# Kernel tuning notes

Measured on AMD Instinct MI355X. Metric: run time of the kernel, lower is better.

The kernel has to match this reference:

```python
import jax, jax.numpy as jnp
import numpy as np

B, S, D, H = 2, 2048, 1024, 16
DK = D // H
NEG = -65504.0  # matches torch masked_fill value in source


def setup_inputs() -> dict:
    key = jax.random.key(0)
    ks = jax.random.split(key, 5)
    scale = 1.0 / np.sqrt(D)
    return {
        "x": jax.random.normal(ks[0], (B, S, D), dtype=jnp.float32),
        "W_q": jax.random.normal(ks[1], (D, D), dtype=jnp.float32) * scale,
        "W_k": jax.random.normal(ks[2], (D, D), dtype=jnp.float32) * scale,
        "W_v": jax.random.normal(ks[3], (D, D), dtype=jnp.float32) * scale,
        "W_o": jax.random.normal(ks[4], (D, D), dtype=jnp.float32) * scale,
    }


def reference(x, W_q, W_k, W_v, W_o):
    b, s, d = x.shape
    # nn.Linear(x) = x @ W.T ; split heads -> [b, h, s, dk]
    def proj(W):
        return (x @ W.T).reshape(b, s, H, DK).transpose(0, 2, 1, 3)
    q, k, v = proj(W_q), proj(W_k), proj(W_v)
    scores = jnp.einsum("bhqd,bhkd->bhqk", q, k) / jnp.sqrt(jnp.float32(DK))
    causal = jnp.tril(jnp.ones((s, s), dtype=bool))  # True where attending allowed
    scores = jnp.where(causal, scores, NEG)
    attn = jax.nn.softmax(scores, axis=-1)  # attn_pdrop=0 -> dropout is identity
    out = jnp.einsum("bhqk,bhkd->bhqd", attn, v)
    out = out.transpose(0, 2, 1, 3).reshape(b, s, d)
    return out @ W_o.T
```

## Files before the change

kernel.cpp:

```cpp
#include <hip/hip_runtime.h>
#include <hip/hip_bf16.h>

typedef __attribute__((ext_vector_type(4))) float f32x4;
typedef __attribute__((ext_vector_type(8))) short bf16x8;

#define Bn 2
#define Sn 2048
#define Dn 1024
#define Hn 16
#define DKn 64
#define Mrows (Bn * Sn)

__device__ __forceinline__ unsigned short f2bf(float f) {
  unsigned int x = __float_as_uint(f);
  x += 0x7fffu + ((x >> 16) & 1u);
  return (unsigned short)(x >> 16);
}

__device__ __forceinline__ float bf2f(unsigned short u) {
  return __uint_as_float(((unsigned int)u) << 16);
}

__device__ __forceinline__ unsigned int cvtpk(float lo, float hi) {
  unsigned int r;
  asm("v_cvt_pk_bf16_f32 %0, %1, %2" : "=v"(r) : "v"(lo), "v"(hi));
  return r;
}

__device__ __forceinline__ float exp2a(float x) {
  float r;
  asm("v_exp_f32 %0, %1" : "=v"(r) : "v"(x));
  return r;
}

__device__ __forceinline__ f32x4 mfma16(bf16x8 a, bf16x8 b, f32x4 c) {
  return __builtin_amdgcn_mfma_f32_16x16x32_bf16(a, b, c, 0, 0, 0);
}

__device__ __forceinline__ f32x4 max4(f32x4 a, f32x4 b) {
  f32x4 r;
  r[0] = fmaxf(a[0], b[0]); r[1] = fmaxf(a[1], b[1]);
  r[2] = fmaxf(a[2], b[2]); r[3] = fmaxf(a[3], b[3]);
  return r;
}

__device__ __forceinline__ void gload_lds16(const unsigned short* g, unsigned short* l) {
  __builtin_amdgcn_global_load_lds(
      (const __attribute__((address_space(1))) void*)g,
      (__attribute__((address_space(3))) void*)l, 16, 0, 0);
}

__global__ __launch_bounds__(256)
void cvt_all(const float* __restrict__ x,  const float* __restrict__ wq,
             const float* __restrict__ wk, const float* __restrict__ wv,
             const float* __restrict__ wo,
             unsigned short* __restrict__ xb,  unsigned short* __restrict__ wqb,
             unsigned short* __restrict__ wkb, unsigned short* __restrict__ wvb,
             unsigned short* __restrict__ wob) {
  int i = (blockIdx.x * 256 + threadIdx.x) * 4;
  const float* src; unsigned short* dst; int off;
  int r = i >> 20;
  if (r < 4)       { src = x;  dst = xb;  off = i; }
  else if (r == 4) { src = wq; dst = wqb; off = i & 1048575; }
  else if (r == 5) { src = wk; dst = wkb; off = i & 1048575; }
  else if (r == 6) { src = wv; dst = wvb; off = i & 1048575; }
  else             { src = wo; dst = wob; off = i & 1048575; }
  float4 v = *(const float4*)(src + off);
  ushort4 o;
  o.x = f2bf(v.x); o.y = f2bf(v.y); o.z = f2bf(v.z); o.w = f2bf(v.w);
  *(ushort4*)(dst + off) = o;
}

template<int MODE>
__device__ __forceinline__ void gemm_body(const unsigned short* __restrict__ A,
                                          const unsigned short* __restrict__ W,
                                          unsigned short* __restrict__ Cb,
                                          float* __restrict__ Cf,
                                          unsigned short* As,
                                          unsigned short* Bs,
                                          int row0, int col0) {
  const int K = Dn, N = Dn;
  const int tid  = threadIdx.x;
  const int wid  = tid >> 6;
  const int lane = tid & 63;
  const int l15  = lane & 15;
  const int lg   = lane >> 4;
  const int wr = (wid >> 1) * 64;
  const int wc = (wid & 1) * 64;

  f32x4 acc[4][4] = {};

  const int lrow2 = lane >> 2;
  const int gs    = (lane & 3) ^ ((lane >> 3) & 3);
  const int swzr  = (l15 >> 1) & 3;

  auto stage = [&](int kt, int b) {
#pragma unroll
    for (int q = 0; q < 2; ++q) {
      int chunk = wid * 2 + q;
      int r = chunk * 16 + lrow2;
      gload_lds16(A + (size_t)(row0 + r) * K + kt + gs * 8,
                  &As[b * 4096 + chunk * 512]);
    }
#pragma unroll
    for (int q = 0; q < 2; ++q) {
      int chunk = wid * 2 + q;
      int r = chunk * 16 + lrow2;
      gload_lds16(W + (size_t)(col0 + r) * K + kt + gs * 8,
                  &Bs[b * 4096 + chunk * 512]);
    }
  };

  auto compute = [&](int b) {
    bf16x8 af[4], bfr[4];
#pragma unroll
    for (int m = 0; m < 4; ++m)
      af[m] = *(const bf16x8*)(&As[b * 4096 + (wr + m * 16 + l15) * 32 +
                                   ((lg ^ swzr) * 8)]);
#pragma unroll
    for (int n = 0; n < 4; ++n)
      bfr[n] = *(const bf16x8*)(&Bs[b * 4096 + (wc + n * 16 + l15) * 32 +
                                    ((lg ^ swzr) * 8)]);
    __builtin_amdgcn_s_setprio(1);
#pragma unroll
    for (int m = 0; m < 4; ++m)
#pragma unroll
      for (int n = 0; n < 4; ++n)
        acc[m][n] = mfma16(af[m], bfr[n], acc[m][n]);
    __builtin_amdgcn_s_setprio(0);
  };

  stage(0, 0);
  stage(32, 1);
  int cb = 0;
#pragma unroll 1
  for (int t = 0; t < 32; ++t) {
    if (t < 31) asm volatile("s_waitcnt vmcnt(4)" ::: "memory");
    else        asm volatile("s_waitcnt vmcnt(0)" ::: "memory");
    __builtin_amdgcn_sched_barrier(0);
    __builtin_amdgcn_s_barrier();
    __builtin_amdgcn_sched_barrier(0);
    if (t <= 29) {
      int sb = cb + 2; if (sb >= 3) sb -= 3;
      stage((t + 2) * 32, sb);
    }
    compute(cb);
    ++cb; if (cb == 3) cb = 0;
  }

#pragma unroll
  for (int m = 0; m < 4; ++m)
#pragma unroll
    for (int n = 0; n < 4; ++n) {
      int r0 = row0 + wr + m * 16 + lg * 4;
      int c  = col0 + wc + n * 16 + l15;
      if (MODE == 2) {
        int b = r0 >> 11, s = r0 & 2047;
        int h = c >> 6,  d = c & 63;
        ushort4 pw;
        pw.x = f2bf(acc[m][n][0]); pw.y = f2bf(acc[m][n][1]);
        pw.z = f2bf(acc[m][n][2]); pw.w = f2bf(acc[m][n][3]);
        *(ushort4*)(Cb + ((((size_t)b * Hn + h) * DKn + d) << 11) + s) = pw;
      } else {
#pragma unroll
        for (int j = 0; j < 4; ++j) {
          size_t idx = (size_t)(r0 + j) * N + c;
          float v = acc[m][n][j];
          if (MODE == 3)      Cf[idx] = v;
          else if (MODE == 0) Cb[idx] = f2bf(v * 0.18033688f);
          else                Cb[idx] = f2bf(v);
        }
      }
    }
}

__global__ __launch_bounds__(256, 3)
void gemm_qkv(const unsigned short* __restrict__ A,
              const unsigned short* __restrict__ W0,
              const unsigned short* __restrict__ W1,
              const unsigned short* __restrict__ W2,
              unsigned short* __restrict__ C0,
              unsigned short* __restrict__ C1,
              unsigned short* __restrict__ C2) {
  __shared__ unsigned short As[3 * 128 * 32];
  __shared__ unsigned short Bs[3 * 128 * 32];
  const int fid = blockIdx.x;
  const int panel = fid % 24;
  const int row0 = (fid / 24) * 128;
  const int col0 = (panel & 7) * 128;
  const int z = panel >> 3;
  if (z == 0)      gemm_body<0>(A, W0, C0, nullptr, As, Bs, row0, col0);
  else if (z == 1) gemm_body<1>(A, W1, C1, nullptr, As, Bs, row0, col0);
  else             gemm_body<2>(A, W2, C2, nullptr, As, Bs, row0, col0);
}

__global__ __launch_bounds__(256, 3)
void gemm_out(const unsigned short* __restrict__ A,
              const unsigned short* __restrict__ W,
              float* __restrict__ C) {
  __shared__ unsigned short As[3 * 128 * 32];
  __shared__ unsigned short Bs[3 * 128 * 32];
  gemm_body<3>(A, W, nullptr, C, As, Bs, blockIdx.x * 128, blockIdx.y * 128);
}

__global__ __launch_bounds__(512, 4)
void attn_part(const unsigned short* __restrict__ Qg,
               const unsigned short* __restrict__ Kg,
               const unsigned short* __restrict__ Vtg,
               unsigned short* __restrict__ Og,
               unsigned short* __restrict__ Pb,
               float* __restrict__ Pml) {
  const int bid = blockIdx.x;
  const int bh = bid & 31;
  const int j  = bid >> 5;
  const int bb = bh >> 4, hh = bh & 15;
  const int tid = threadIdx.x, wid = tid >> 6, lane = tid & 63;
  const int l15 = lane & 15, lg = lane >> 4;
  const int wq = wid * 16;
  const size_t baseQ = (size_t)bb * Sn * Dn + (size_t)hh * DKn;
  const size_t baseV = (size_t)bh * DKn * Sn;

  __shared__ unsigned short Ks[2][64 * 64];
  __shared__ unsigned short Vts[3][64 * 64];
  __shared__ unsigned short Ps[8][16 * 72];

  const int lrow  = lane >> 3;
  const int sgran = (lane & 7) ^ lrow;
  const int swz   = l15 & 7;

  const int g0 = 17 * j;
  int qtC = 0;
  while ((qtC + 1) * (qtC + 2) <= g0) ++qtC;
  int ktC = g0 - qtC * (qtC + 1);
  int qtN = qtC, ktN = ktC;
  { ++ktN; if (ktN == 2 * qtN + 2) { ktN = 0; ++qtN; } }
  int sqt = qtC, skt = ktC;
  int snum = 0;

  auto stage = [&]() {
    const int k0 = skt << 6;
    const int ksl = snum & 1, vsl = snum % 3;
    gload_lds16(Kg + baseQ + (size_t)(k0 + wid * 8 + lrow) * Dn + sgran * 8,
                &Ks[ksl][wid * 512]);
    gload_lds16(Vtg + baseV + (size_t)(wid * 8 + lrow) * Sn + k0 + sgran * 8,
                &Vts[vsl][wid * 512]);
    ++snum;
    ++skt; if (skt == 2 * sqt + 2) { skt = 0; ++sqt; }
  };

  bf16x8 qf[2];
  auto loadQ = [&](int qtile) {
    const int q0 = qtile * 128;
#pragma unroll
    for (int kd = 0; kd < 2; ++kd)
      qf[kd] = *(const bf16x8*)(Qg + baseQ +
               (size_t)(q0 + wq + l15) * Dn + kd * 32 + lg * 8);
  };

  f32x4 sfA[4], sfB[4];
  f32x4 oacc[4] = {};
  float mrun = -1e30f;
  float lrun = 0.f;
  int pstart = ktC;

  stage(); stage();
  loadQ(qtC);
  asm volatile("s_waitcnt vmcnt(0)" ::: "memory");
  __builtin_amdgcn_sched_barrier(0);
  __builtin_amdgcn_s_barrier();
  if ((ktC << 6) <= qtC * 128 + wq + 15) {
#pragma unroll
    for (int kn = 0; kn < 4; ++kn) sfA[kn] = f32x4{0.f, 0.f, 0.f, 0.f};
    __builtin_amdgcn_s_setprio(1);
#pragma unroll
    for (int kn = 0; kn < 4; ++kn)
#pragma unroll
      for (int kd = 0; kd < 2; ++kd) {
        bf16x8 kf = *(const bf16x8*)(&Ks[0][(kn * 16 + l15) * 64 +
                                          (((kd * 4 + lg) ^ swz) * 8)]);
        sfA[kn] = mfma16(kf, qf[kd], sfA[kn]);
      }
    __builtin_amdgcn_s_setprio(0);
  }

  auto body = [&](int i, f32x4 (&sfC)[4], f32x4 (&sfN)[4]) {
    asm volatile("s_waitcnt vmcnt(0)" ::: "memory");
    __builtin_amdgcn_sched_barrier(0);
    __builtin_amdgcn_s_barrier();
    if (i <= 14) stage();

    if (i < 16) {
      if (ktN == 0) loadQ(qtN);
      const int k0n = ktN << 6;
      if (k0n <= qtN * 128 + wq + 15) {
        const int ksl = (i + 1) & 1;
#pragma unroll
        for (int kn = 0; kn < 4; ++kn) sfN[kn] = f32x4{0.f, 0.f, 0.f, 0.f};
        __builtin_amdgcn_s_setprio(1);
#pragma unroll
        for (int kn = 0; kn < 4; ++kn)
#pragma unroll
          for (int kd = 0; kd < 2; ++kd) {
            bf16x8 kf = *(const bf16x8*)(&Ks[ksl][(kn * 16 + l15) * 64 +
                                                 (((kd * 4 + lg) ^ swz) * 8)]);
            sfN[kn] = mfma16(kf, qf[kd], sfN[kn]);
          }
        __builtin_amdgcn_s_setprio(0);
      }
    }

    const int k0c = ktC << 6;
    const int q0c = qtC * 128;
    if (k0c <= q0c + wq + 15) {
      if (k0c + 63 > q0c + wq) {
        int qq = q0c + wq + l15;
#pragma unroll
        for (int kn = 0; kn < 4; ++kn)
#pragma unroll
          for (int jj = 0; jj < 4; ++jj) {
            int key = k0c + kn * 16 + lg * 4 + jj;
            if (key > qq) sfC[kn][jj] = -1e30f;
          }
      }
      f32x4 mm = max4(max4(sfC[0], sfC[1]), max4(sfC[2], sfC[3]));
      float tl = fmaxf(fmaxf(mm[0], mm[1]), fmaxf(mm[2], mm[3]));
      if (__any(tl > mrun + 11.5f)) {
        float t = tl;
        t = fmaxf(t, __shfl_xor(t, 16));
        t = fmaxf(t, __shfl_xor(t, 32));
        float mnew = fmaxf(mrun, t);
        float corr = exp2a(mrun - mnew);
        mrun = mnew;
        lrun *= corr;
#pragma unroll
        for (int dn = 0; dn < 4; ++dn) oacc[dn] *= corr;
      }
      const float m = mrun;
#pragma unroll
      for (int kn = 0; kn < 4; ++kn) {
#pragma unroll
        for (int jj = 0; jj < 4; ++jj)
          sfC[kn][jj] = exp2a(sfC[kn][jj] - m);
        uint2 pw;
        pw.x = cvtpk(sfC[kn][0], sfC[kn][1]);
        pw.y = cvtpk(sfC[kn][2], sfC[kn][3]);
        *(uint2*)(&Ps[wid][l15 * 72 + kn * 16 + lg * 4]) = pw;
      }
      f32x4 sv = (sfC[0] + sfC[1]) + (sfC[2] + sfC[3]);
      lrun += (sv[0] + sv[1]) + (sv[2] + sv[3]);

      const int vsl = i % 3;
      __builtin_amdgcn_s_setprio(1);
#pragma unroll
      for (int kk = 0; kk < 2; ++kk) {
        bf16x8 pf = *(const bf16x8*)(&Ps[wid][l15 * 72 + kk * 32 + lg * 8]);
#pragma unroll
        for (int dn = 0; dn < 4; ++dn) {
          bf16x8 vf = *(const bf16x8*)(&Vts[vsl][(dn * 16 + l15) * 64 +
                                                (((kk * 4 + lg) ^ swz) * 8)]);
          oacc[dn] = mfma16(vf, pf, oacc[dn]);
        }
      }
      __builtin_amdgcn_s_setprio(0);
    }

    const bool segend = (ktC == 2 * qtC + 1);
    if (segend || i == 16) {
      if (pstart == 0 && segend) {
        float lt = lrun;
        lt += __shfl_xor(lt, 16);
        lt += __shfl_xor(lt, 32);
        float rinv = 1.0f / lt;
        int row = q0c + wq + l15;
#pragma unroll
        for (int dn = 0; dn < 4; ++dn) {
          ushort4 ow;
          ow.x = f2bf(oacc[dn][0] * rinv);
          ow.y = f2bf(oacc[dn][1] * rinv);
          ow.z = f2bf(oacc[dn][2] * rinv);
          ow.w = f2bf(oacc[dn][3] * rinv);
          *(ushort4*)(Og + baseQ + (size_t)row * Dn + dn * 16 + lg * 4) = ow;
        }
      } else {
        const int seg_s = qtC * (qtC + 1);
        const int ord = pstart ? ((seg_s + pstart) / 17 - seg_s / 17) : 0;
        const size_t slot = (size_t)((bh * 16 + qtC) * 3 + ord);
        float lt = lrun;
        lt += __shfl_xor(lt, 16);
        lt += __shfl_xor(lt, 32);
        int rl = wq + l15;
#pragma unroll
        for (int dn = 0; dn < 4; ++dn) {
          ushort4 ow;
          ow.x = f2bf(oacc[dn][0]);
          ow.y = f2bf(oacc[dn][1]);
          ow.z = f2bf(oacc[dn][2]);
          ow.w = f2bf(oacc[dn][3]);
          *(ushort4*)(Pb + slot * 8192 + (size_t)rl * 64 + dn * 16 + lg * 4) = ow;
        }
        if (lg == 0) {
          Pml[slot * 256 + rl] = mrun;
          Pml[slot * 256 + 128 + rl] = lt;
        }
      }
      if (i < 16) {
        pstart = 0;
        mrun = -1e30f; lrun = 0.f;
#pragma unroll
        for (int dn = 0; dn < 4; ++dn) oacc[dn] = f32x4{0.f, 0.f, 0.f, 0.f};
      }
    }
    qtC = qtN; ktC = ktN;
    ++ktN; if (ktN == 2 * qtN + 2) { ktN = 0; ++qtN; }
  };

#pragma unroll 1
  for (int i = 0; i < 17; i += 2) {
    body(i, sfA, sfB);
    if (i + 1 < 17) body(i + 1, sfB, sfA);
  }
}

__global__ __launch_bounds__(256)
void attn_combine(const unsigned short* __restrict__ Pb,
                  const float* __restrict__ Pml,
                  unsigned short* __restrict__ Og) {
  const int bid = blockIdx.x;
  const int qt = bid >> 5, bh = bid & 31;
  const int b = bh * 16 + qt;
  const int seg_s = qt * (qt + 1);
  const int seg_e = seg_s + 2 * qt + 2;
  const int c0 = (seg_s / 17 + 1) * 17;
  if (c0 >= seg_e) return;
  const int np = (c0 + 17 < seg_e) ? 3 : 2;
  const int bb = bh >> 4, hh = bh & 15;
  const size_t baseQ = (size_t)bb * Sn * Dn + (size_t)hh * DKn;
  const int q0 = qt * 128;
  const int slot0 = b * 3;
  const int r = threadIdx.x >> 1;
  const int c32 = (threadIdx.x & 1) * 32;

  float m0 = Pml[(size_t)slot0 * 256 + r];
  float l0 = Pml[(size_t)slot0 * 256 + 128 + r];
  float m1 = Pml[(size_t)(slot0 + 1) * 256 + r];
  float l1 = Pml[(size_t)(slot0 + 1) * 256 + 128 + r];
  float m2 = -1e30f, l2 = 0.f;
  if (np == 3) {
    m2 = Pml[(size_t)(slot0 + 2) * 256 + r];
    l2 = Pml[(size_t)(slot0 + 2) * 256 + 128 + r];
  }
  float M = fmaxf(fmaxf(m0, m1), m2);
  float w0 = exp2a(m0 - M), w1 = exp2a(m1 - M);
  float w2 = (np == 3) ? exp2a(m2 - M) : 0.f;
  float L = l0 * w0 + l1 * w1 + l2 * w2;

  float acc[32];
#pragma unroll
  for (int k = 0; k < 32; ++k) acc[k] = 0.f;

  auto accum = [&](int p, float w) {
    const unsigned short* src = Pb + (size_t)(slot0 + p) * 8192 + (size_t)r * 64 + c32;
#pragma unroll
    for (int k4 = 0; k4 < 8; ++k4) {
      ushort4 v = *(const ushort4*)(src + k4 * 4);
      acc[k4 * 4 + 0] += w * bf2f(v.x);
      acc[k4 * 4 + 1] += w * bf2f(v.y);
      acc[k4 * 4 + 2] += w * bf2f(v.z);
      acc[k4 * 4 + 3] += w * bf2f(v.w);
    }
  };
  accum(0, w0);
  accum(1, w1);
  if (np == 3) accum(2, w2);

  float rinv = 1.0f / L;
#pragma unroll
  for (int k4 = 0; k4 < 8; ++k4) {
    ushort4 o;
    o.x = f2bf(acc[k4 * 4 + 0] * rinv);
    o.y = f2bf(acc[k4 * 4 + 1] * rinv);
    o.z = f2bf(acc[k4 * 4 + 2] * rinv);
    o.w = f2bf(acc[k4 * 4 + 3] * rinv);
    *(ushort4*)(Og + baseQ + (size_t)(q0 + r) * Dn + c32 + k4 * 4) = o;
  }
}

extern "C" void kernel_launch(void* const* d_in, const int* in_sizes, int n_in,
                              void* d_out, int out_size, void* d_ws, size_t ws_size,
                              hipStream_t stream) {
  const float* x  = (const float*)d_in[0];
  const float* Wq = (const float*)d_in[1];
  const float* Wk = (const float*)d_in[2];
  const float* Wv = (const float*)d_in[3];
  const float* Wo = (const float*)d_in[4];
  float* out = (float*)d_out;

  char* ws = (char*)d_ws;
  size_t off = 0;
  unsigned short* xb  = (unsigned short*)(ws + off); off += (size_t)Mrows * Dn * 2;
  unsigned short* wqb = (unsigned short*)(ws + off); off += (size_t)Dn * Dn * 2;
  unsigned short* wkb = (unsigned short*)(ws + off); off += (size_t)Dn * Dn * 2;
  unsigned short* wvb = (unsigned short*)(ws + off); off += (size_t)Dn * Dn * 2;
  unsigned short* wob = (unsigned short*)(ws + off); off += (size_t)Dn * Dn * 2;
  unsigned short* Qb  = (unsigned short*)(ws + off); off += (size_t)Mrows * Dn * 2;
  unsigned short* Kb  = (unsigned short*)(ws + off); off += (size_t)Mrows * Dn * 2;
  unsigned short* Vtb = (unsigned short*)(ws + off); off += (size_t)Mrows * Dn * 2;
  unsigned short* Ob  = (unsigned short*)(ws + off); off += (size_t)Mrows * Dn * 2;
  unsigned short* Pb  = (unsigned short*)(ws + off); off += (size_t)1536 * 8192 * 2;
  float*          Pml = (float*)(ws + off);          off += (size_t)1536 * 256 * 4;

  cvt_all<<<8192, 256, 0, stream>>>(x, Wq, Wk, Wv, Wo, xb, wqb, wkb, wvb, wob);
  gemm_qkv<<<768, 256, 0, stream>>>(xb, wqb, wkb, wvb, Qb, Kb, Vtb);
  attn_part<<<512, 512, 0, stream>>>(Qb, Kb, Vtb, Ob, Pb, Pml);
  attn_combine<<<512, 256, 0, stream>>>(Pb, Pml, Ob);
  gemm_out<<<dim3(Mrows / 128, Dn / 128), 256, 0, stream>>>(Ob, wob, out);
}
```

Before: 109.2 us.

## Replace QKV GEMM with 256x256-tile 8-wave ping-pong kernel over concatenated weights

The QKV projection now runs in one kernel with 256x256 output tiles, 512 threads and a 64-wide K step. It relies on the Q, K and V weight buffers sitting next to each other in the workspace, so they act as one 3072-row weight matrix. The main loop is hand-interleaved: LDS fragment reads, global-to-LDS staging, explicit barriers and waitcnts, with s_setprio raised around MFMA bursts so memory traffic overlaps math. The aim is more data reuse per tile and better overlap of loads with compute. The cost is only 192 workgroups, fewer than the CU count, and heavy LDS and register use per block.

After: 111.6 us. 1.02x slower.

```diff
diff --git a/kernel.cpp b/kernel.cpp
--- a/kernel.cpp
+++ b/kernel.cpp
@@ -49,6 +49,11 @@
       (const __attribute__((address_space(1))) void*)g,
       (__attribute__((address_space(3))) void*)l, 16, 0, 0);
 }
+
+#define SBAR()  do { __builtin_amdgcn_sched_barrier(0); __builtin_amdgcn_s_barrier(); __builtin_amdgcn_sched_barrier(0); } while (0)
+#define LGKM0() do { asm volatile("s_waitcnt lgkmcnt(0)" ::: "memory"); __builtin_amdgcn_sched_barrier(0); } while (0)
+#define VMC6()  do { asm volatile("s_waitcnt vmcnt(6)" ::: "memory"); __builtin_amdgcn_sched_barrier(0); } while (0)
+#define VMC0()  do { asm volatile("s_waitcnt vmcnt(0)" ::: "memory"); __builtin_amdgcn_sched_barrier(0); } while (0)
 
 __global__ __launch_bounds__(256)
 void cvt_all(const float* __restrict__ x,  const float* __restrict__ wq,
@@ -71,20 +76,227 @@
   *(ushort4*)(dst + off) = o;
 }
 
-template<int MODE>
-__device__ __forceinline__ void gemm_body(const unsigned short* __restrict__ A,
-                                          const unsigned short* __restrict__ W,
-                                          unsigned short* __restrict__ Cb,
-                                          float* __restrict__ Cf,
-                                          unsigned short* As,
-                                          unsigned short* Bs,
-                                          int row0, int col0) {
+__global__ __launch_bounds__(512, 2)
+void gemm_qkv8(const unsigned short* __restrict__ A,
+               const unsigned short* __restrict__ Wcat,
+               unsigned short* __restrict__ Cq,
+               unsigned short* __restrict__ Ck,
+               unsigned short* __restrict__ Cv) {
+  __shared__ unsigned short As[2 * 256 * 64];
+  __shared__ unsigned short Bs[2 * 256 * 64];
+  const int bid  = blockIdx.x;
+  const int row0 = (bid / 12) * 256;
+  const int col0 = (bid % 12) * 256;
+  const int K    = Dn;
+  const int tid  = threadIdx.x;
+  const int wid  = tid >> 6;
+  const int lane = tid & 63;
+  const int l15  = lane & 15;
+  const int lg   = lane >> 4;
+  const int lrow = lane >> 3;
+  const int sgran = (lane & 7) ^ lrow;
+  const int wm = (wid >> 2) * 128;
+  const int wn = (wid & 3) * 64;
+
+  auto stageA = [&](int kt, int h) {
+    const int slot = kt & 1;
+#pragma unroll
+    for (int q = 0; q < 2; ++q) {
+      int c  = wid * 2 + q;
+      int lr = (c >> 3) * 128 + h * 64 + (c & 7) * 8;
+      gload_lds16(A + (size_t)(row0 + lr + lrow) * K + kt * 64 + sgran * 8,
+                  &As[slot * 16384 + lr * 64]);
+    }
+  };
+  auto stageB = [&](int kt, int h) {
+    const int slot = kt & 1;
+#pragma unroll
+    for (int q = 0; q < 2; ++q) {
+      int c  = wid * 2 + q;
+      int lr = (c >> 2) * 64 + h * 32 + (c & 3) * 8;
+      gload_lds16(Wcat + (size_t)(col0 + lr + lrow) * K + kt * 64 + sgran * 8,
+                  &Bs[slot * 16384 + lr * 64]);
+    }
+  };
+  auto rdA = [&](int slot, int mi, int kk) -> bf16x8 {
+    int row = wm + mi * 16 + l15;
+    return *(const bf16x8*)(&As[slot * 16384 + row * 64 +
+                                (((kk * 4 + lg) ^ (l15 & 7)) * 8)]);
+  };
+  auto rdB = [&](int slot, int ni, int kk) -> bf16x8 {
+    int row = wn + ni * 16 + l15;
+    return *(const bf16x8*)(&Bs[slot * 16384 + row * 64 +
+                                (((kk * 4 + lg) ^ (l15 & 7)) * 8)]);
+  };
+
+  f32x4 acc[8][4] = {};
+  bf16x8 af[4][2];
+  bf16x8 bf[4][2];
+
+  stageA(0, 0); stageB(0, 0); stageB(0, 1); stageA(0, 1);
+  stageA(1, 0); stageB(1, 0); stageB(1, 1);
+  VMC6();
+  SBAR();
+
+#pragma unroll 1
+  for (int it = 0; it < 8; ++it) {
+    const int t2 = 2 * it + 2, t3 = 2 * it + 3;
+
+#pragma unroll
+    for (int mi = 0; mi < 4; ++mi) { af[mi][0] = rdA(0, mi, 0); af[mi][1] = rdA(0, mi, 1); }
+#pragma unroll
+    for (int ni = 0; ni < 2; ++ni) { bf[ni][0] = rdB(0, ni, 0); bf[ni][1] = rdB(0, ni, 1); }
+    stageA(2 * it + 1, 1);
+    SBAR(); LGKM0();
+    __builtin_amdgcn_s_setprio(1);
+#pragma unroll
+    for (int mi = 0; mi < 4; ++mi)
+#pragma unroll
+      for (int ni = 0; ni < 2; ++ni) {
+        acc[mi][ni] = mfma16(af[mi][0], bf[ni][0], acc[mi][ni]);
+        acc[mi][ni] = mfma16(af[mi][1], bf[ni][1], acc[mi][ni]);
+      }
+    __builtin_amdgcn_s_setprio(0);
+    SBAR();
+#pragma unroll
+    for (int ni = 2; ni < 4; ++ni) { bf[ni][0] = rdB(0, ni, 0); bf[ni][1] = rdB(0, ni, 1); }
+    if (t2 < 16) stageA(t2, 0);
+    SBAR(); LGKM0();
+    __builtin_amdgcn_s_setprio(1);
+#pragma unroll
+    for (int mi = 0; mi < 4; ++mi)
+#pragma unroll
+      for (int ni = 2; ni < 4; ++ni) {
+        acc[mi][ni] = mfma16(af[mi][0], bf[ni][0], acc[mi][ni]);
+        acc[mi][ni] = mfma16(af[mi][1], bf[ni][1], acc[mi][ni]);
+      }
+    __builtin_amdgcn_s_setprio(0);
+    SBAR();
+#pragma unroll
+    for (int mi = 0; mi < 4; ++mi) { af[mi][0] = rdA(0, mi + 4, 0); af[mi][1] = rdA(0, mi + 4, 1); }
+    if (t2 < 16) stageB(t2, 0);
+    SBAR(); LGKM0();
+    __builtin_amdgcn_s_setprio(1);
+#pragma unroll
+    for (int mi = 0; mi < 4; ++mi)
+#pragma unroll
+      for (int ni = 0; ni < 2; ++ni) {
+        acc[mi + 4][ni] = mfma16(af[mi][0], bf[ni][0], acc[mi + 4][ni]);
+        acc[mi + 4][ni] = mfma16(af[mi][1], bf[ni][1], acc[mi + 4][ni]);
+      }
+    __builtin_amdgcn_s_setprio(0);
+    SBAR();
+    if (t2 < 16) stageB(t2, 1);
+    if (it == 7) { VMC0(); } else { VMC6(); }
+    SBAR();
+    __builtin_amdgcn_s_setprio(1);
+#pragma unroll
+    for (int mi = 0; mi < 4; ++mi)
+#pragma unroll
+      for (int ni = 2; ni < 4; ++ni) {
+        acc[mi + 4][ni] = mfma16(af[mi][0], bf[ni][0], acc[mi + 4][ni]);
+        acc[mi + 4][ni] = mfma16(af[mi][1], bf[ni][1], acc[mi + 4][ni]);
+      }
+    __builtin_amdgcn_s_setprio(0);
+    SBAR();
+#pragma unroll
+    for (int mi = 0; mi < 4; ++mi) { af[mi][0] = rdA(1, mi, 0); af[mi][1] = rdA(1, mi, 1); }
+#pragma unroll
+    for (int ni = 0; ni < 2; ++ni) { bf[ni][0] = rdB(1, ni, 0); bf[ni][1] = rdB(1, ni, 1); }
+    if (t2 < 16) stageA(t2, 1);
+    SBAR(); LGKM0();
+    __builtin_amdgcn_s_setprio(1);
+#pragma unroll
+    for (int mi = 0; mi < 4; ++mi)
+#pragma unroll
+      for (int ni = 0; ni < 2; ++ni) {
+        acc[mi][ni] = mfma16(af[mi][0], bf[ni][0], acc[mi][ni]);
+        acc[mi][ni] = mfma16(af[mi][1], bf[ni][1], acc[mi][ni]);
+      }
+    __builtin_amdgcn_s_setprio(0);
+    SBAR();
+#pragma unroll
+    for (int ni = 2; ni < 4; ++ni) { bf[ni][0] = rdB(1, ni, 0); bf[ni][1] = rdB(1, ni, 1); }
+    if (t3 < 16) stageA(t3, 0);
+    SBAR(); LGKM0();
+    __builtin_amdgcn_s_setprio(1);
+#pragma unroll
+    for (int mi = 0; mi < 4; ++mi)
+#pragma unroll
+      for (int ni = 2; ni < 4; ++ni) {
+        acc[mi][ni] = mfma16(af[mi][0], bf[ni][0], acc[mi][ni]);
+        acc[mi][ni] = mfma16(af[mi][1], bf[ni][1], acc[mi][ni]);
+      }
+    __builtin_amdgcn_s_setprio(0);
+    SBAR();
+#pragma unroll
+    for (int mi = 0; mi < 4; ++mi) { af[mi][0] = rdA(1, mi + 4, 0); af[mi][1] = rdA(1, mi + 4, 1); }
+    if (t3 < 16) stageB(t3, 0);
+    SBAR(); LGKM0();
+    __builtin_amdgcn_s_setprio(1);
+#pragma unroll
+    for (int mi = 0; mi < 4; ++mi)
+#pragma unroll
+      for (int ni = 0; ni < 2; ++ni) {
+        acc[mi + 4][ni] = mfma16(af[mi][0], bf[ni][0], acc[mi + 4][ni]);
+        acc[mi + 4][ni] = mfma16(af[mi][1], bf[ni][1], acc[mi + 4][ni]);
+      }
+    __builtin_amdgcn_s_setprio(0);
+    SBAR();
+    if (t3 < 16) stageB(t3, 1);
+    if (it < 7) { VMC6(); }
+    SBAR();
+    __builtin_amdgcn_s_setprio(1);
+#pragma unroll
+    for (int mi = 0; mi < 4; ++mi)
+#pragma unroll
+      for (int ni = 2; ni < 4; ++ni) {
+        acc[mi + 4][ni] = mfma16(af[mi][0], bf[ni][0], acc[mi + 4][ni]);
+        acc[mi + 4][ni] = mfma16(af[mi][1], bf[ni][1], acc[mi + 4][ni]);
+      }
+    __builtin_amdgcn_s_setprio(0);
+    SBAR();
+  }
+
+  const int z   = col0 >> 10;
+  const int cl0 = col0 & 1023;
+#pragma unroll
+  for (int mi = 0; mi < 8; ++mi)
+#pragma unroll
+    for (int ni = 0; ni < 4; ++ni) {
+      int r0 = row0 + wm + mi * 16 + lg * 4;
+      int c  = cl0 + wn + ni * 16 + l15;
+      if (z == 2) {
+        int b = r0 >> 11, s = r0 & 2047;
+        int h = c >> 6,  d = c & 63;
+        ushort4 pw;
+        pw.x = f2bf(acc[mi][ni][0]); pw.y = f2bf(acc[mi][ni][1]);
+        pw.z = f2bf(acc[mi][ni][2]); pw.w = f2bf(acc[mi][ni][3]);
+        *(ushort4*)(Cv + ((((size_t)b * Hn + h) * DKn + d) << 11) + s) = pw;
+      } else {
+        unsigned short* C = (z == 0) ? Cq : Ck;
+        const float sc = (z == 0) ? 0.18033688f : 1.0f;
+#pragma unroll
+        for (int jj = 0; jj < 4; ++jj)
+          C[(size_t)(r0 + jj) * Dn + c] = f2bf(acc[mi][ni][jj] * sc);
+      }
+    }
+}
+
+__global__ __launch_bounds__(256, 3)
+void gemm_out(const unsigned short* __restrict__ A,
+              const unsigned short* __restrict__ W,
+              float* __restrict__ C) {
+  __shared__ unsigned short As[3 * 128 * 32];
+  __shared__ unsigned short Bs[3 * 128 * 32];
   const int K = Dn, N = Dn;
   const int tid  = threadIdx.x;
   const int wid  = tid >> 6;
   const int lane = tid & 63;
   const int l15  = lane & 15;
   const int lg   = lane >> 4;
+  const int row0 = blockIdx.x * 128;
+  const int col0 = blockIdx.y * 128;
   const int wr = (wid >> 1) * 64;
   const int wc = (wid & 1) * 64;
 
@@ -154,53 +366,10 @@
     for (int n = 0; n < 4; ++n) {
       int r0 = row0 + wr + m * 16 + lg * 4;
       int c  = col0 + wc + n * 16 + l15;
-      if (MODE == 2) {
-        int b = r0 >> 11, s = r0 & 2047;
-        int h = c >> 6,  d = c & 63;
-        ushort4 pw;
-        pw.x = f2bf(acc[m][n][0]); pw.y = f2bf(acc[m][n][1]);
-        pw.z = f2bf(acc[m][n][2]); pw.w = f2bf(acc[m][n][3]);
-        *(ushort4*)(Cb + ((((size_t)b * Hn + h) * DKn + d) << 11) + s) = pw;
-      } else {
-#pragma unroll
-        for (int j = 0; j < 4; ++j) {
-          size_t idx = (size_t)(r0 + j) * N + c;
-          float v = acc[m][n][j];
-          if (MODE == 3)      Cf[idx] = v;
-          else if (MODE == 0) Cb[idx] = f2bf(v * 0.18033688f);
-          else                Cb[idx] = f2bf(v);
-        }
-      }
-    }
-}
-
-__global__ __launch_bounds__(256, 3)
-void gemm_qkv(const unsigned short* __restrict__ A,
-              const unsigned short* __restrict__ W0,
-              const unsigned short* __restrict__ W1,
-              const unsigned short* __restrict__ W2,
-              unsigned short* __restrict__ C0,
-              unsigned short* __restrict__ C1,
-              unsigned short* __restrict__ C2) {
-  __shared__ unsigned short As[3 * 128 * 32];
-  __shared__ unsigned short Bs[3 * 128 * 32];
-  const int fid = blockIdx.x;
-  const int panel = fid % 24;
-  const int row0 = (fid / 24) * 128;
-  const int col0 = (panel & 7) * 128;
-  const int z = panel >> 3;
-  if (z == 0)      gemm_body<0>(A, W0, C0, nullptr, As, Bs, row0, col0);
-  else if (z == 1) gemm_body<1>(A, W1, C1, nullptr, As, Bs, row0, col0);
-  else             gemm_body<2>(A, W2, C2, nullptr, As, Bs, row0, col0);
-}
-
-__global__ __launch_bounds__(256, 3)
-void gemm_out(const unsigned short* __restrict__ A,
-              const unsigned short* __restrict__ W,
-              float* __restrict__ C) {
-  __shared__ unsigned short As[3 * 128 * 32];
-  __shared__ unsigned short Bs[3 * 128 * 32];
-  gemm_body<3>(A, W, nullptr, C, As, Bs, blockIdx.x * 128, blockIdx.y * 128);
+#pragma unroll
+      for (int j = 0; j < 4; ++j)
+        C[(size_t)(r0 + j) * N + c] = acc[m][n][j];
+    }
 }
 
 __global__ __launch_bounds__(512, 4)
@@ -510,7 +679,7 @@
   float*          Pml = (float*)(ws + off);          off += (size_t)1536 * 256 * 4;
 
   cvt_all<<<8192, 256, 0, stream>>>(x, Wq, Wk, Wv, Wo, xb, wqb, wkb, wvb, wob);
-  gemm_qkv<<<768, 256, 0, stream>>>(xb, wqb, wkb, wvb, Qb, Kb, Vtb);
+  gemm_qkv8<<<192, 512, 0, stream>>>(xb, wqb, Qb, Kb, Vtb);
   attn_part<<<512, 512, 0, stream>>>(Qb, Kb, Vtb, Ob, Pb, Pml);
   attn_combine<<<512, 256, 0, stream>>>(Pb, Pml, Ob);
   gemm_out<<<dim3(Mrows / 128, Dn / 128), 256, 0, stream>>>(Ob, wob, out);
```
